# Optimization experiments

Hardware: AMD Instinct MI355X
Metric: run time of the kernel (lower is better)

## Reference

```python
import jax, jax.numpy as jnp
import numpy as np

K_BITS = 4
V_BITS = 4
GROUP_SIZE = 64
EPS = 1e-8


def _quant_dequant_per_token(x, bits):
    # TurboQuantProd: symmetric per-token (per head_dim vector) absmax quantization.
    qmax = 2.0 ** (bits - 1) - 1.0
    scale = jnp.maximum(jnp.max(jnp.abs(x), axis=-1, keepdims=True) / qmax, EPS)
    return jnp.clip(jnp.round(x / scale), -qmax, qmax) * scale


def _quant_dequant_grouped(x, bits, group_size):
    # TurboQuantValue: symmetric grouped absmax quantization along head_dim.
    shp = x.shape
    xg = x.reshape(shp[:-1] + (shp[-1] // group_size, group_size))
    qmax = 2.0 ** (bits - 1) - 1.0
    scale = jnp.maximum(jnp.max(jnp.abs(xg), axis=-1, keepdims=True) / qmax, EPS)
    dq = jnp.clip(jnp.round(xg / scale), -qmax, qmax) * scale
    return dq.reshape(shp)


def setup_inputs() -> dict:
    key = jax.random.key(0)
    kq, kk, kv = jax.random.split(key, 3)
    B, H, S, D = 2, 16, 2048, 128
    query = jax.random.normal(kq, (B, H, S, D), dtype=jnp.float32)
    k = jax.random.normal(kk, (B, H, S, D), dtype=jnp.float32)
    v = jax.random.normal(kv, (B, H, S, D), dtype=jnp.float32)
    causal_mask = jnp.tril(jnp.ones((S, S), dtype=bool))[None, None]  # [1,1,S,S]
    return {"query": query, "key": k, "value": v, "causal_mask": causal_mask}


def reference(query, key, value, causal_mask):
    # Non-protected path: quantize K per-token, V grouped, then fused dequant + SDPA.
    head_dim = query.shape[-1]
    scale = 1.0 / np.sqrt(head_dim).astype(np.float32)
    dq_key = _quant_dequant_per_token(key, K_BITS)
    dq_value = _quant_dequant_grouped(value, V_BITS, GROUP_SIZE)
    scores = jnp.einsum('bhqd,bhkd->bhqk', query, dq_key) * scale
    scores = jnp.where(causal_mask, scores, -jnp.inf)
    weights = jax.nn.softmax(scores, axis=-1)
    output = jnp.einsum('bhqk,bhkd->bhqd', weights, dq_value)
    return (output, weights)
```

## Files before the change

### kernel.cpp

```cpp
#include <hip/hip_runtime.h>

#define SQ 2048
#define DD 128
#define BHN 32
#define SC2 0.12751741934f

typedef __attribute__((ext_vector_type(8))) short bf16x8;
typedef __attribute__((ext_vector_type(4))) float f32x4;

__device__ __forceinline__ unsigned cvtpk(float a, float b){
  unsigned r;
  asm("v_cvt_pk_bf16_f32 %0, %1, %2" : "=v"(r) : "v"(a), "v"(b));
  return r;
}
union U8 { unsigned u[4]; bf16x8 h; };

__device__ __forceinline__ void gl_lds16(const void* g, void* l){
  __builtin_amdgcn_global_load_lds(
      (const __attribute__((address_space(1))) unsigned int*)g,
      (__attribute__((address_space(3))) unsigned int*)l, 16, 0, 0);
}

__global__ __launch_bounds__(256) void qd_kernel(const float* __restrict__ K,
                                                 const float* __restrict__ V,
                                                 char* __restrict__ dqK,
                                                 char* __restrict__ dqVt){
  __shared__ float Vlds[128*65];
  const int t = threadIdx.x;
  const int bh = blockIdx.x >> 5;
  const int stile = blockIdx.x & 31;
  const int tt = t >> 2;
  const int q4 = t & 3;
  const int s = stile*64 + tt;
  const long ebase = ((long)(bh*SQ + s))*DD + 32*q4;

  float vals[32];
  {
    const float4* kp = (const float4*)(K + ebase);
    float am = 0.f;
    #pragma unroll
    for (int j=0;j<8;j++){
      float4 v4 = kp[j];
      vals[4*j+0]=v4.x; vals[4*j+1]=v4.y; vals[4*j+2]=v4.z; vals[4*j+3]=v4.w;
      am = fmaxf(am, fmaxf(fmaxf(fabsf(v4.x),fabsf(v4.y)),fmaxf(fabsf(v4.z),fabsf(v4.w))));
    }
    am = fmaxf(am, __shfl_xor(am,1));
    am = fmaxf(am, __shfl_xor(am,2));
    const float sc = fmaxf(am/7.0f, 1e-8f);
    #pragma unroll
    for (int j=0;j<32;j++){
      float qv = rintf(vals[j]/sc);
      qv = fminf(7.f, fmaxf(-7.f, qv));
      vals[j] = qv*sc;
    }
    const long rowb = ((long)(bh*SQ + s))*256;
    const int swz = (s & 7) << 4;
    #pragma unroll
    for (int c=0;c<4;c++){
      uint4 w;
      w.x = cvtpk(vals[8*c+0], vals[8*c+1]);
      w.y = cvtpk(vals[8*c+2], vals[8*c+3]);
      w.z = cvtpk(vals[8*c+4], vals[8*c+5]);
      w.w = cvtpk(vals[8*c+6], vals[8*c+7]);
      *(uint4*)(dqK + rowb + ((64*q4 + 16*c) ^ swz)) = w;
    }
  }
  {
    const float4* vp = (const float4*)(V + ebase);
    float am = 0.f;
    #pragma unroll
    for (int j=0;j<8;j++){
      float4 v4 = vp[j];
      vals[4*j+0]=v4.x; vals[4*j+1]=v4.y; vals[4*j+2]=v4.z; vals[4*j+3]=v4.w;
      am = fmaxf(am, fmaxf(fmaxf(fabsf(v4.x),fabsf(v4.y)),fmaxf(fabsf(v4.z),fabsf(v4.w))));
    }
    am = fmaxf(am, __shfl_xor(am,1));
    const float sc = fmaxf(am/7.0f, 1e-8f);
    #pragma unroll
    for (int j=0;j<32;j++){
      float qv = rintf(vals[j]/sc);
      qv = fminf(7.f, fmaxf(-7.f, qv));
      Vlds[(32*q4 + j)*65 + tt] = qv*sc;
    }
  }
  __syncthreads();
  #pragma unroll
  for (int m=0;m<4;m++){
    const int chunk = m*256 + t;
    const int d = chunk >> 3;
    const int c = chunk & 7;
    uint4 w;
    const float* f = &Vlds[d*65 + 8*c];
    w.x = cvtpk(f[0], f[1]);
    w.y = cvtpk(f[2], f[3]);
    w.z = cvtpk(f[4], f[5]);
    w.w = cvtpk(f[6], f[7]);
    const long ob = ((long)(bh*DD + d))*4096 + (long)stile*128 + ((16*c) ^ ((d&7)<<4));
    *(uint4*)(dqVt + ob) = w;
  }
}

__global__ __launch_bounds__(256,2) void attn_fused(const float* __restrict__ Q,
    const char* __restrict__ dqK, const char* __restrict__ dqVt,
    float* __restrict__ Out, float* __restrict__ Wout){
  __shared__ __attribute__((aligned(16))) char Kt[2][16384];
  __shared__ __attribute__((aligned(16))) char Vt[2][16384];
  __shared__ __attribute__((aligned(16))) char Et[4][4096];

  const int bid = blockIdx.x;
  const int xcd = bid & 7;
  const int loc = bid >> 3;
  const int bh  = xcd*4 + (loc & 3);
  const int i   = loc >> 2;
  const int p   = (i < 8) ? i : (23 - i);
  const int t = threadIdx.x;
  const int lane = t & 63;
  const int w = t >> 6;
  const int l15 = lane & 15, l4 = lane >> 4;
  const int swz = (l15 & 7) << 4;

  const int qtA = 31 - p, qtB = p;
  const int q0A = qtA*64, q0B = qtB*64;
  const int nktA = qtA + 1;
  const int nktB = qtB + 1;
  const int rA = q0A + 16*w + l15;
  const int rB = q0B + 16*w + l15;

  bf16x8 qa[2][4];
  #pragma unroll
  for (int g=0; g<2; ++g){
    const int qrow = g ? rB : rA;
    const float* qb = Q + ((long)(bh*SQ) + qrow)*DD + 8*l4;
    #pragma unroll
    for (int kk=0;kk<4;kk++){
      float4 a = *(const float4*)(qb + 32*kk);
      float4 b = *(const float4*)(qb + 32*kk + 4);
      U8 cv;
      cv.u[0] = cvtpk(a.x*SC2, a.y*SC2);
      cv.u[1] = cvtpk(a.z*SC2, a.w*SC2);
      cv.u[2] = cvtpk(b.x*SC2, b.y*SC2);
      cv.u[3] = cvtpk(b.z*SC2, b.w*SC2);
      qa[g][kk] = cv.h;
    }
  }

  const char* Kb = dqK + (long)bh*SQ*256;
  const char* Vb = dqVt + (long)bh*DD*4096;

  const f32x4 z4 = {0.f,0.f,0.f,0.f};
  f32x4 oacc[2][8] = {{z4,z4,z4,z4,z4,z4,z4,z4},{z4,z4,z4,z4,z4,z4,z4,z4}};
  float ssum[2] = {0.f, 0.f};
  char* eb = &Et[w][0];

  auto stageKV = [&](int buf, int kt){
    const char* ks = Kb + (long)kt*16384;
    #pragma unroll
    for (int it=0;it<4;it++)
      gl_lds16(ks + it*4096 + t*16, &Kt[buf][it*4096 + t*16]);
    const char* vs = Vb + (long)kt*128;
    #pragma unroll
    for (int it=0;it<4;it++)
      gl_lds16(vs + (long)(it*32 + (t>>3))*4096 + (t&7)*16, &Vt[buf][it*4096 + t*16]);
  };

  stageKV(0, 0);
  __syncthreads();
  int cur = 0;
  for (int kt=0; kt<nktA; ++kt){
    if (kt+1 < nktA) stageKV(cur^1, kt+1);
    const bool doB = (kt < nktB);
    const int k0 = kt*64;

    f32x4 sacc[2][4] = {{z4,z4,z4,z4},{z4,z4,z4,z4}};
    {
      const char* kbase = &Kt[cur][0] + l15*256;
      __builtin_amdgcn_s_setprio(1);
      if (doB){
        #pragma unroll
        for (int cf=0;cf<4;cf++){
          #pragma unroll
          for (int kk=0;kk<4;kk++){
            bf16x8 kb = *(const bf16x8*)(kbase + cf*4096 + ((64*kk+16*l4) ^ swz));
            sacc[0][cf] = __builtin_amdgcn_mfma_f32_16x16x32_bf16(kb, qa[0][kk], sacc[0][cf], 0,0,0);
            sacc[1][cf] = __builtin_amdgcn_mfma_f32_16x16x32_bf16(kb, qa[1][kk], sacc[1][cf], 0,0,0);
          }
        }
      } else {
        #pragma unroll
        for (int cf=0;cf<4;cf++){
          #pragma unroll
          for (int kk=0;kk<4;kk++){
            bf16x8 kb = *(const bf16x8*)(kbase + cf*4096 + ((64*kk+16*l4) ^ swz));
            sacc[0][cf] = __builtin_amdgcn_mfma_f32_16x16x32_bf16(kb, qa[0][kk], sacc[0][cf], 0,0,0);
          }
        }
      }
      __builtin_amdgcn_s_setprio(0);
    }

    {
      if (kt < qtA){
        #pragma unroll
        for (int cf=0;cf<4;cf++){
          float e0 = exp2f(sacc[0][cf][0]);
          float e1 = exp2f(sacc[0][cf][1]);
          float e2 = exp2f(sacc[0][cf][2]);
          float e3 = exp2f(sacc[0][cf][3]);
          ssum[0] += (e0+e1) + (e2+e3);
          uint2 wp; wp.x = cvtpk(e0,e1); wp.y = cvtpk(e2,e3);
          *(uint2*)(eb + l15*128 + ((32*cf + 8*l4) ^ swz)) = wp;
        }
      } else {
        #pragma unroll
        for (int cf=0;cf<4;cf++){
          const int tok0 = k0 + 16*cf + 4*l4;
          float e0 = (tok0+0 <= rA) ? exp2f(sacc[0][cf][0]) : 0.f;
          float e1 = (tok0+1 <= rA) ? exp2f(sacc[0][cf][1]) : 0.f;
          float e2 = (tok0+2 <= rA) ? exp2f(sacc[0][cf][2]) : 0.f;
          float e3 = (tok0+3 <= rA) ? exp2f(sacc[0][cf][3]) : 0.f;
          ssum[0] += (e0+e1) + (e2+e3);
          uint2 wp; wp.x = cvtpk(e0,e1); wp.y = cvtpk(e2,e3);
          *(uint2*)(eb + l15*128 + ((32*cf + 8*l4) ^ swz)) = wp;
        }
      }
    }
    if (doB){
      const int lr = 16 + l15;
      if (kt < qtB){
        #pragma unroll
        for (int cf=0;cf<4;cf++){
          float e0 = exp2f(sacc[1][cf][0]);
          float e1 = exp2f(sacc[1][cf][1]);
          float e2 = exp2f(sacc[1][cf][2]);
          float e3 = exp2f(sacc[1][cf][3]);
          ssum[1] += (e0+e1) + (e2+e3);
          uint2 wp; wp.x = cvtpk(e0,e1); wp.y = cvtpk(e2,e3);
          *(uint2*)(eb + lr*128 + ((32*cf + 8*l4) ^ swz)) = wp;
        }
      } else {
        #pragma unroll
        for (int cf=0;cf<4;cf++){
          const int tok0 = k0 + 16*cf + 4*l4;
          float e0 = (tok0+0 <= rB) ? exp2f(sacc[1][cf][0]) : 0.f;
          float e1 = (tok0+1 <= rB) ? exp2f(sacc[1][cf][1]) : 0.f;
          float e2 = (tok0+2 <= rB) ? exp2f(sacc[1][cf][2]) : 0.f;
          float e3 = (tok0+3 <= rB) ? exp2f(sacc[1][cf][3]) : 0.f;
          ssum[1] += (e0+e1) + (e2+e3);
          uint2 wp; wp.x = cvtpk(e0,e1); wp.y = cvtpk(e2,e3);
          *(uint2*)(eb + lr*128 + ((32*cf + 8*l4) ^ swz)) = wp;
        }
      }
    }

    {
      const char* vbase = &Vt[cur][0] + l15*128;
      __builtin_amdgcn_s_setprio(1);
      if (doB){
        #pragma unroll
        for (int kc=0;kc<2;kc++){
          const int eo = (64*kc + 16*l4) ^ swz;
          bf16x8 ea0 = *(const bf16x8*)(eb + l15*128 + eo);
          bf16x8 ea1 = *(const bf16x8*)(eb + (16+l15)*128 + eo);
          #pragma unroll
          for (int df=0;df<8;df++){
            bf16x8 vv = *(const bf16x8*)(vbase + df*2048 + eo);
            oacc[0][df] = __builtin_amdgcn_mfma_f32_16x16x32_bf16(ea0, vv, oacc[0][df], 0,0,0);
            oacc[1][df] = __builtin_amdgcn_mfma_f32_16x16x32_bf16(ea1, vv, oacc[1][df], 0,0,0);
          }
        }
      } else {
        #pragma unroll
        for (int kc=0;kc<2;kc++){
          const int eo = (64*kc + 16*l4) ^ swz;
          bf16x8 ea0 = *(const bf16x8*)(eb + l15*128 + eo);
          #pragma unroll
          for (int df=0;df<8;df++){
            bf16x8 vv = *(const bf16x8*)(vbase + df*2048 + eo);
            oacc[0][df] = __builtin_amdgcn_mfma_f32_16x16x32_bf16(ea0, vv, oacc[0][df], 0,0,0);
          }
        }
      }
      __builtin_amdgcn_s_setprio(0);
    }
    __syncthreads();
    cur ^= 1;
  }

  float si[2];
  #pragma unroll
  for (int g=0; g<2; ++g){
    float sm = ssum[g];
    sm += __shfl_xor(sm, 16);
    sm += __shfl_xor(sm, 32);
    si[g] = 1.0f / sm;
    float invr[4];
    #pragma unroll
    for (int ii=0;ii<4;ii++) invr[ii] = __shfl(si[g], 4*l4+ii);
    const int rb0 = (g ? q0B : q0A) + 16*w;
    float* ob = Out + ((long)(bh*SQ) + rb0)*DD;
    #pragma unroll
    for (int df=0;df<8;df++){
      #pragma unroll
      for (int ii=0;ii<4;ii++)
        ob[(4*l4+ii)*DD + 16*df + l15] = oacc[g][df][ii]*invr[ii];
    }
  }

  float* Wbase = Wout + (long)bh*SQ*SQ;
  float* wrowA = Wbase + (long)rA*SQ;
  float* wrowB = Wbase + (long)rB*SQ;

  for (int kt=0; kt<nktA; ++kt){
    const int k0 = kt*64;
    const char* kr = Kb + (long)kt*16384 + l15*256;
    const bool doB = (kt < nktB);

    bf16x8 kb[4][4];
    #pragma unroll
    for (int cf=0;cf<4;cf++){
      #pragma unroll
      for (int kk=0;kk<4;kk++)
        kb[cf][kk] = *(const bf16x8*)(kr + cf*4096 + ((64*kk+16*l4) ^ swz));
    }

    f32x4 sacc[2][4] = {{z4,z4,z4,z4},{z4,z4,z4,z4}};
    __builtin_amdgcn_s_setprio(1);
    if (doB){
      #pragma unroll
      for (int cf=0;cf<4;cf++){
        #pragma unroll
        for (int kk=0;kk<4;kk++){
          sacc[0][cf] = __builtin_amdgcn_mfma_f32_16x16x32_bf16(kb[cf][kk], qa[0][kk], sacc[0][cf], 0,0,0);
          sacc[1][cf] = __builtin_amdgcn_mfma_f32_16x16x32_bf16(kb[cf][kk], qa[1][kk], sacc[1][cf], 0,0,0);
        }
      }
    } else {
      #pragma unroll
      for (int cf=0;cf<4;cf++){
        #pragma unroll
        for (int kk=0;kk<4;kk++)
          sacc[0][cf] = __builtin_amdgcn_mfma_f32_16x16x32_bf16(kb[cf][kk], qa[0][kk], sacc[0][cf], 0,0,0);
      }
    }
    __builtin_amdgcn_s_setprio(0);

    if (kt < qtA){
      #pragma unroll
      for (int cf=0;cf<4;cf++){
        const int tok0 = k0 + 16*cf + 4*l4;
        f32x4 wv;
        wv[0] = exp2f(sacc[0][cf][0])*si[0];
        wv[1] = exp2f(sacc[0][cf][1])*si[0];
        wv[2] = exp2f(sacc[0][cf][2])*si[0];
        wv[3] = exp2f(sacc[0][cf][3])*si[0];
        *(f32x4*)(wrowA + tok0) = wv;
      }
    } else {
      #pragma unroll
      for (int cf=0;cf<4;cf++){
        const int tok0 = k0 + 16*cf + 4*l4;
        f32x4 wv;
        wv[0] = (tok0+0 <= rA) ? exp2f(sacc[0][cf][0])*si[0] : 0.f;
        wv[1] = (tok0+1 <= rA) ? exp2f(sacc[0][cf][1])*si[0] : 0.f;
        wv[2] = (tok0+2 <= rA) ? exp2f(sacc[0][cf][2])*si[0] : 0.f;
        wv[3] = (tok0+3 <= rA) ? exp2f(sacc[0][cf][3])*si[0] : 0.f;
        *(f32x4*)(wrowA + tok0) = wv;
      }
    }
    if (doB){
      if (kt < qtB){
        #pragma unroll
        for (int cf=0;cf<4;cf++){
          const int tok0 = k0 + 16*cf + 4*l4;
          f32x4 wv;
          wv[0] = exp2f(sacc[1][cf][0])*si[1];
          wv[1] = exp2f(sacc[1][cf][1])*si[1];
          wv[2] = exp2f(sacc[1][cf][2])*si[1];
          wv[3] = exp2f(sacc[1][cf][3])*si[1];
          *(f32x4*)(wrowB + tok0) = wv;
        }
      } else {
        #pragma unroll
        for (int cf=0;cf<4;cf++){
          const int tok0 = k0 + 16*cf + 4*l4;
          f32x4 wv;
          wv[0] = (tok0+0 <= rB) ? exp2f(sacc[1][cf][0])*si[1] : 0.f;
          wv[1] = (tok0+1 <= rB) ? exp2f(sacc[1][cf][1])*si[1] : 0.f;
          wv[2] = (tok0+2 <= rB) ? exp2f(sacc[1][cf][2])*si[1] : 0.f;
          wv[3] = (tok0+3 <= rB) ? exp2f(sacc[1][cf][3])*si[1] : 0.f;
          *(f32x4*)(wrowB + tok0) = wv;
        }
      }
    }
  }

  const f32x4 zz = {0.f,0.f,0.f,0.f};
  {
    const int z0 = nktA*64;
    for (int rr=0; rr<16 && z0 < SQ; rr++){
      float* row = Wbase + (long)(q0A + 16*w + rr)*SQ;
      for (int c = z0 + 4*lane; c < SQ; c += 256)
        *(f32x4*)(row + c) = zz;
    }
  }
  {
    const int z0 = nktB*64;
    for (int rr=0; rr<16; rr++){
      float* row = Wbase + (long)(q0B + 16*w + rr)*SQ;
      for (int c = z0 + 4*lane; c < SQ; c += 256)
        *(f32x4*)(row + c) = zz;
    }
  }
}

extern "C" void kernel_launch(void* const* d_in, const int* in_sizes, int n_in,
                              void* d_out, int out_size, void* d_ws, size_t ws_size,
                              hipStream_t stream) {
  const float* Q = (const float*)d_in[0];
  const float* K = (const float*)d_in[1];
  const float* V = (const float*)d_in[2];
  float* Out = (float*)d_out;
  float* Wout = (float*)d_out + (size_t)BHN*SQ*DD;
  char* dqK  = (char*)d_ws;
  char* dqVt = (char*)d_ws + (size_t)BHN*SQ*DD*2;

  qd_kernel<<<BHN*32, 256, 0, stream>>>(K, V, dqK, dqVt);
  attn_fused<<<512, 256, 0, stream>>>(Q, dqK, dqVt, Out, Wout);
}
```

Before: 226.3 us.

## Use 32-token KV tiles with triple-buffered LDS and per-warp causal tile skipping

The first pass now steps through K/V in 32-token tiles instead of 64, with a three-stage LDS ring and explicit vmcnt waits plus barriers, replacing the double buffer and __syncthreads. Each warp checks where its 16 rows sit against the tile and skips QK/PV MFMAs for tiles that are fully masked, applying the causal mask only on diagonal tiles. The V and E LDS layouts and swizzles are reworked to match the smaller tiles. This cuts wasted causal work and deepens prefetch, at the cost of more loop iterations, more barriers and divergent per-warp control flow.

```diff
diff --git a/kernel.cpp b/kernel.cpp
--- a/kernel.cpp
+++ b/kernel.cpp
@@ -103,9 +103,9 @@
 __global__ __launch_bounds__(256,2) void attn_fused(const float* __restrict__ Q,
     const char* __restrict__ dqK, const char* __restrict__ dqVt,
     float* __restrict__ Out, float* __restrict__ Wout){
-  __shared__ __attribute__((aligned(16))) char Kt[2][16384];
-  __shared__ __attribute__((aligned(16))) char Vt[2][16384];
-  __shared__ __attribute__((aligned(16))) char Et[4][4096];
+  __shared__ __attribute__((aligned(16))) char Kt[3][8192];
+  __shared__ __attribute__((aligned(16))) char Vt[3][8192];
+  __shared__ __attribute__((aligned(16))) char Et[4][2560];
 
   const int bid = blockIdx.x;
   const int xcd = bid & 7;
@@ -121,10 +121,11 @@
 
   const int qtA = 31 - p, qtB = p;
   const int q0A = qtA*64, q0B = qtB*64;
-  const int nktA = qtA + 1;
-  const int nktB = qtB + 1;
-  const int rA = q0A + 16*w + l15;
-  const int rB = q0B + 16*w + l15;
+  const int rb0 = q0A + 16*w;
+  const int rb1 = q0B + 16*w;
+  const int rA = rb0 + l15;
+  const int rB = rb1 + l15;
+  const int nkt = 2*qtA + 2;
 
   bf16x8 qa[2][4];
   #pragma unroll
@@ -152,138 +153,112 @@
   float ssum[2] = {0.f, 0.f};
   char* eb = &Et[w][0];
 
-  auto stageKV = [&](int buf, int kt){
-    const char* ks = Kb + (long)kt*16384;
-    #pragma unroll
-    for (int it=0;it<4;it++)
-      gl_lds16(ks + it*4096 + t*16, &Kt[buf][it*4096 + t*16]);
-    const char* vs = Vb + (long)kt*128;
-    #pragma unroll
-    for (int it=0;it<4;it++)
-      gl_lds16(vs + (long)(it*32 + (t>>3))*4096 + (t&7)*16, &Vt[buf][it*4096 + t*16]);
+  auto stage = [&](int b, int kt){
+    const char* ks = Kb + (long)kt*8192;
+    gl_lds16(ks + t*16,        &Kt[b][t*16]);
+    gl_lds16(ks + 4096 + t*16, &Kt[b][4096 + t*16]);
+    const int k0b = kt*64;
+    #pragma unroll
+    for (int it=0; it<2; ++it){
+      const int c = t + 256*it;
+      const int row = c >> 2, pos = c & 3;
+      const long so = (long)row*4096 + (long)((k0b + 16*(pos ^ (row&3))) ^ ((row&7)<<4));
+      gl_lds16(Vb + so, &Vt[b][c*16]);
+    }
   };
 
-  stageKV(0, 0);
-  __syncthreads();
-  int cur = 0;
-  for (int kt=0; kt<nktA; ++kt){
-    if (kt+1 < nktA) stageKV(cur^1, kt+1);
-    const bool doB = (kt < nktB);
-    const int k0 = kt*64;
-
-    f32x4 sacc[2][4] = {{z4,z4,z4,z4},{z4,z4,z4,z4}};
+  stage(0, 0);
+  stage(1, 1);
+  int bc = 0;
+  for (int kt=0; kt<nkt; ++kt){
+    if (kt+1 < nkt) asm volatile("s_waitcnt vmcnt(4)\n\ts_barrier" ::: "memory");
+    else            asm volatile("s_waitcnt vmcnt(0)\n\ts_barrier" ::: "memory");
     {
-      const char* kbase = &Kt[cur][0] + l15*256;
-      __builtin_amdgcn_s_setprio(1);
-      if (doB){
+      int bs = bc + 2; if (bs >= 3) bs -= 3;
+      if (kt+2 < nkt) stage(bs, kt+2);
+    }
+
+    const int tk0 = 32*kt;
+    const int st0 = (tk0+31 <= rb0) ? 2 : ((tk0 <= rb0+15) ? 1 : 0);
+    const int st1 = (tk0+31 <= rb1) ? 2 : ((tk0 <= rb1+15) ? 1 : 0);
+
+    if (st0){
+      f32x4 sacc[2][2] = {{z4,z4},{z4,z4}};
+      {
+        const char* kbase = &Kt[bc][0] + l15*256;
+        __builtin_amdgcn_s_setprio(1);
+        if (st1){
+          #pragma unroll
+          for (int cf=0;cf<2;cf++){
+            #pragma unroll
+            for (int kk=0;kk<4;kk++){
+              bf16x8 kb = *(const bf16x8*)(kbase + cf*4096 + ((64*kk+16*l4) ^ swz));
+              sacc[0][cf] = __builtin_amdgcn_mfma_f32_16x16x32_bf16(kb, qa[0][kk], sacc[0][cf], 0,0,0);
+              sacc[1][cf] = __builtin_amdgcn_mfma_f32_16x16x32_bf16(kb, qa[1][kk], sacc[1][cf], 0,0,0);
+            }
+          }
+        } else {
+          #pragma unroll
+          for (int cf=0;cf<2;cf++){
+            #pragma unroll
+            for (int kk=0;kk<4;kk++){
+              bf16x8 kb = *(const bf16x8*)(kbase + cf*4096 + ((64*kk+16*l4) ^ swz));
+              sacc[0][cf] = __builtin_amdgcn_mfma_f32_16x16x32_bf16(kb, qa[0][kk], sacc[0][cf], 0,0,0);
+            }
+          }
+        }
+        __builtin_amdgcn_s_setprio(0);
+      }
+
+      #pragma unroll
+      for (int g=0; g<2; ++g){
+        const int st = g ? st1 : st0;
+        if (!st) continue;
+        const int r  = g ? rB : rA;
+        const int lr = 16*g + l15;
         #pragma unroll
-        for (int cf=0;cf<4;cf++){
-          #pragma unroll
-          for (int kk=0;kk<4;kk++){
-            bf16x8 kb = *(const bf16x8*)(kbase + cf*4096 + ((64*kk+16*l4) ^ swz));
-            sacc[0][cf] = __builtin_amdgcn_mfma_f32_16x16x32_bf16(kb, qa[0][kk], sacc[0][cf], 0,0,0);
-            sacc[1][cf] = __builtin_amdgcn_mfma_f32_16x16x32_bf16(kb, qa[1][kk], sacc[1][cf], 0,0,0);
+        for (int cf=0;cf<2;cf++){
+          const int tok0 = tk0 + 16*cf + 4*l4;
+          float e0,e1,e2,e3;
+          if (st == 2){
+            e0 = exp2f(sacc[g][cf][0]); e1 = exp2f(sacc[g][cf][1]);
+            e2 = exp2f(sacc[g][cf][2]); e3 = exp2f(sacc[g][cf][3]);
+          } else {
+            e0 = (tok0+0 <= r) ? exp2f(sacc[g][cf][0]) : 0.f;
+            e1 = (tok0+1 <= r) ? exp2f(sacc[g][cf][1]) : 0.f;
+            e2 = (tok0+2 <= r) ? exp2f(sacc[g][cf][2]) : 0.f;
+            e3 = (tok0+3 <= r) ? exp2f(sacc[g][cf][3]) : 0.f;
           }
-        }
-      } else {
-        #pragma unroll
-        for (int cf=0;cf<4;cf++){
-          #pragma unroll
-          for (int kk=0;kk<4;kk++){
-            bf16x8 kb = *(const bf16x8*)(kbase + cf*4096 + ((64*kk+16*l4) ^ swz));
-            sacc[0][cf] = __builtin_amdgcn_mfma_f32_16x16x32_bf16(kb, qa[0][kk], sacc[0][cf], 0,0,0);
-          }
-        }
-      }
-      __builtin_amdgcn_s_setprio(0);
-    }
-
-    {
-      if (kt < qtA){
-        #pragma unroll
-        for (int cf=0;cf<4;cf++){
-          float e0 = exp2f(sacc[0][cf][0]);
-          float e1 = exp2f(sacc[0][cf][1]);
-          float e2 = exp2f(sacc[0][cf][2]);
-          float e3 = exp2f(sacc[0][cf][3]);
-          ssum[0] += (e0+e1) + (e2+e3);
+          ssum[g] += (e0+e1) + (e2+e3);
           uint2 wp; wp.x = cvtpk(e0,e1); wp.y = cvtpk(e2,e3);
-          *(uint2*)(eb + l15*128 + ((32*cf + 8*l4) ^ swz)) = wp;
-        }
-      } else {
-        #pragma unroll
-        for (int cf=0;cf<4;cf++){
-          const int tok0 = k0 + 16*cf + 4*l4;
-          float e0 = (tok0+0 <= rA) ? exp2f(sacc[0][cf][0]) : 0.f;
-          float e1 = (tok0+1 <= rA) ? exp2f(sacc[0][cf][1]) : 0.f;
-          float e2 = (tok0+2 <= rA) ? exp2f(sacc[0][cf][2]) : 0.f;
-          float e3 = (tok0+3 <= rA) ? exp2f(sacc[0][cf][3]) : 0.f;
-          ssum[0] += (e0+e1) + (e2+e3);
-          uint2 wp; wp.x = cvtpk(e0,e1); wp.y = cvtpk(e2,e3);
-          *(uint2*)(eb + l15*128 + ((32*cf + 8*l4) ^ swz)) = wp;
-        }
-      }
-    }
-    if (doB){
-      const int lr = 16 + l15;
-      if (kt < qtB){
-        #pragma unroll
-        for (int cf=0;cf<4;cf++){
-          float e0 = exp2f(sacc[1][cf][0]);
-          float e1 = exp2f(sacc[1][cf][1]);
-          float e2 = exp2f(sacc[1][cf][2]);
-          float e3 = exp2f(sacc[1][cf][3]);
-          ssum[1] += (e0+e1) + (e2+e3);
-          uint2 wp; wp.x = cvtpk(e0,e1); wp.y = cvtpk(e2,e3);
-          *(uint2*)(eb + lr*128 + ((32*cf + 8*l4) ^ swz)) = wp;
-        }
-      } else {
-        #pragma unroll
-        for (int cf=0;cf<4;cf++){
-          const int tok0 = k0 + 16*cf + 4*l4;
-          float e0 = (tok0+0 <= rB) ? exp2f(sacc[1][cf][0]) : 0.f;
-          float e1 = (tok0+1 <= rB) ? exp2f(sacc[1][cf][1]) : 0.f;
-          float e2 = (tok0+2 <= rB) ? exp2f(sacc[1][cf][2]) : 0.f;
-          float e3 = (tok0+3 <= rB) ? exp2f(sacc[1][cf][3]) : 0.f;
-          ssum[1] += (e0+e1) + (e2+e3);
-          uint2 wp; wp.x = cvtpk(e0,e1); wp.y = cvtpk(e2,e3);
-          *(uint2*)(eb + lr*128 + ((32*cf + 8*l4) ^ swz)) = wp;
-        }
-      }
-    }
-
-    {
-      const char* vbase = &Vt[cur][0] + l15*128;
-      __builtin_amdgcn_s_setprio(1);
-      if (doB){
-        #pragma unroll
-        for (int kc=0;kc<2;kc++){
-          const int eo = (64*kc + 16*l4) ^ swz;
-          bf16x8 ea0 = *(const bf16x8*)(eb + l15*128 + eo);
-          bf16x8 ea1 = *(const bf16x8*)(eb + (16+l15)*128 + eo);
+          *(uint2*)(eb + lr*80 + 32*cf + 8*l4) = wp;
+        }
+      }
+
+      {
+        const char* vb2 = &Vt[bc][0] + l15*64;
+        const int eov = (16*l4) ^ ((l15 & 3) << 4);
+        __builtin_amdgcn_s_setprio(1);
+        bf16x8 ea0 = *(const bf16x8*)(eb + l15*80 + 16*l4);
+        if (st1){
+          bf16x8 ea1 = *(const bf16x8*)(eb + (16+l15)*80 + 16*l4);
           #pragma unroll
           for (int df=0;df<8;df++){
-            bf16x8 vv = *(const bf16x8*)(vbase + df*2048 + eo);
+            bf16x8 vv = *(const bf16x8*)(vb2 + df*1024 + eov);
             oacc[0][df] = __builtin_amdgcn_mfma_f32_16x16x32_bf16(ea0, vv, oacc[0][df], 0,0,0);
             oacc[1][df] = __builtin_amdgcn_mfma_f32_16x16x32_bf16(ea1, vv, oacc[1][df], 0,0,0);
           }
-        }
-      } else {
-        #pragma unroll
-        for (int kc=0;kc<2;kc++){
-          const int eo = (64*kc + 16*l4) ^ swz;
-          bf16x8 ea0 = *(const bf16x8*)(eb + l15*128 + eo);
+        } else {
           #pragma unroll
           for (int df=0;df<8;df++){
-            bf16x8 vv = *(const bf16x8*)(vbase + df*2048 + eo);
+            bf16x8 vv = *(const bf16x8*)(vb2 + df*1024 + eov);
             oacc[0][df] = __builtin_amdgcn_mfma_f32_16x16x32_bf16(ea0, vv, oacc[0][df], 0,0,0);
           }
         }
-      }
-      __builtin_amdgcn_s_setprio(0);
-    }
-    __syncthreads();
-    cur ^= 1;
+        __builtin_amdgcn_s_setprio(0);
+      }
+    }
+    bc = bc + 1; if (bc >= 3) bc -= 3;
   }
 
   float si[2];
@@ -296,8 +271,8 @@
     float invr[4];
     #pragma unroll
     for (int ii=0;ii<4;ii++) invr[ii] = __shfl(si[g], 4*l4+ii);
-    const int rb0 = (g ? q0B : q0A) + 16*w;
-    float* ob = Out + ((long)(bh*SQ) + rb0)*DD;
+    const int rbg = g ? rb1 : rb0;
+    float* ob = Out + ((long)(bh*SQ) + rbg)*DD;
     #pragma unroll
     for (int df=0;df<8;df++){
       #pragma unroll
@@ -306,6 +281,7 @@
     }
   }
 
+  const int nktA = qtA + 1, nktB = qtB + 1;
   float* Wbase = Wout + (long)bh*SQ*SQ;
   float* wrowA = Wbase + (long)rA*SQ;
   float* wrowB = Wbase + (long)rB*SQ;
@@ -398,7 +374,7 @@
   {
     const int z0 = nktA*64;
     for (int rr=0; rr<16 && z0 < SQ; rr++){
-      float* row = Wbase + (long)(q0A + 16*w + rr)*SQ;
+      float* row = Wbase + (long)(rb0 + rr)*SQ;
       for (int c = z0 + 4*lane; c < SQ; c += 256)
         *(f32x4*)(row + c) = zz;
     }
@@ -406,7 +382,7 @@
   {
     const int z0 = nktB*64;
     for (int rr=0; rr<16; rr++){
-      float* row = Wbase + (long)(q0B + 16*w + rr)*SQ;
+      float* row = Wbase + (long)(rb1 + rr)*SQ;
       for (int c = z0 + 4*lane; c < SQ; c += 256)
         *(f32x4*)(row + c) = zz;
     }
```

After: 234.1 us. 3.4% more time.
